# Performance work log

Measured on AMD Instinct MI355X. Metric: run time of the kernel, lower is better.

The kernel has to match this reference:

```python
import jax, jax.numpy as jnp
import numpy as np

N_HEADS = 8

def setup_inputs() -> dict:
    key = jax.random.key(0)
    qkv = jax.random.normal(key, (4, 1536, 2048), dtype=jnp.float32)
    return {"qkv": qkv}

def reference(qkv):
    bs, width, length = qkv.shape
    ch = width // (3 * N_HEADS)
    q, k, v = jnp.split(qkv, 3, axis=1)  # each [bs, H*C, T]
    scale = 1.0 / np.sqrt(ch).astype(np.float32)
    q = (q * scale).reshape(bs * N_HEADS, ch, length)
    k = k.reshape(bs * N_HEADS, ch, length)
    v = v.reshape(bs * N_HEADS, ch, length)
    weight = jnp.einsum('bct,bcs->bts', q, k)  # [bs*H, T, T]
    weight = jax.nn.softmax(weight.astype(jnp.float32), axis=-1).astype(weight.dtype)
    a = jnp.einsum('bts,bcs->bct', weight, v)  # [bs*H, C, T]
    return a.reshape(bs, -1, length)
```

## Files before the change

kernel.cpp:

```cpp
#include <hip/hip_runtime.h>
#include <hip/hip_bf16.h>

typedef unsigned short u16;
typedef unsigned int uint;
typedef __bf16 bf16x8 __attribute__((ext_vector_type(8)));
typedef float f32x16 __attribute__((ext_vector_type(16)));

#define SEQ 2048
#define DH  64

__device__ __forceinline__ u16 f2bf(float x) {
  __bf16 h = (__bf16)x;
  return __builtin_bit_cast(u16, h);
}

#define FSW(r) ((((r) & 3) << 1) | (((r) >> 2) & 1))

__global__ __launch_bounds__(256) void transpose_qk(const float* __restrict__ qkv,
                                                    u16* __restrict__ qT,
                                                    u16* __restrict__ kT) {
  int idx = blockIdx.x;
  int which = idx >> 10;
  int bh = (idx >> 5) & 31;
  int t0 = (idx & 31) * 64;
  int b = bh >> 3, h = bh & 7;
  const float* src = qkv + ((size_t)(b*1536 + which*512 + h*64)) * SEQ;
  u16* dst = (which ? kT : qT) + (size_t)bh * SEQ * DH;
  float scale = which ? 1.0f : 0.1803368801111244f;

  __shared__ float tile[64][65];
  int tl = threadIdx.x & 63;
  int cw = threadIdx.x >> 6;
#pragma unroll
  for (int i = 0; i < 16; ++i) {
    int c = cw + 4*i;
    tile[c][tl] = src[(size_t)c*SEQ + t0 + tl] * scale;
  }
  __syncthreads();
  int cl2 = (threadIdx.x & 31) * 2;
  int tw  = threadIdx.x >> 5;
#pragma unroll
  for (int i = 0; i < 8; ++i) {
    int t = tw + 8*i;
    unsigned int lo = f2bf(tile[cl2][t]);
    unsigned int hi = f2bf(tile[cl2+1][t]);
    *(unsigned int*)(dst + (size_t)(t0 + t)*DH + cl2) = lo | (hi << 16);
  }
}

__global__ __launch_bounds__(256) void convert_v(const float* __restrict__ qkv,
                                                 u16* __restrict__ v) {
  int row = blockIdx.x;
  int bh = row >> 6, c = row & 63;
  int b = bh >> 3, h = bh & 7;
  const float4* src = (const float4*)(qkv + ((size_t)(b*1536 + 1024 + h*64 + c)) * SEQ);
  u16* dst = v + (size_t)row * SEQ;
  int tid = threadIdx.x;
  float4 a = src[tid*2];
  float4 bq = src[tid*2+1];
  union { u16 u[8]; int4 v4; } pk;
  pk.u[0]=f2bf(a.x); pk.u[1]=f2bf(a.y); pk.u[2]=f2bf(a.z); pk.u[3]=f2bf(a.w);
  pk.u[4]=f2bf(bq.x); pk.u[5]=f2bf(bq.y); pk.u[6]=f2bf(bq.z); pk.u[7]=f2bf(bq.w);
  *(int4*)(dst + tid*8) = pk.v4;
}

__global__ __launch_bounds__(256) void attn(const u16* __restrict__ qT,
                                            const u16* __restrict__ kT,
                                            const u16* __restrict__ vB,
                                            float* __restrict__ out) {
  const int lb = (blockIdx.x & 7) * 64 + (blockIdx.x >> 3);
  const int bh = lb >> 4;
  const int t0 = (lb & 15) * 128;
  const int tid  = threadIdx.x;
  const int wave = tid >> 6;
  const int lane = tid & 63;
  const int l31  = lane & 31;
  const int hi   = lane >> 5;

  __shared__ __align__(16) u16 kbuf[2][2][64*64];
  __shared__ __align__(16) u16 vbuf[2][2][64*64];

  const u16* qrow = qT + ((size_t)bh*SEQ + (t0 + wave*32 + l31)) * DH;
  bf16x8 bq[4];
#pragma unroll
  for (int kb = 0; kb < 4; ++kb) bq[kb] = *(const bf16x8*)(qrow + kb*16 + hi*8);

  const u16* ksrc0 = kT + (size_t)bh*SEQ*DH;
  const u16* vsrc0 = vB + (size_t)bh*DH*SEQ;
  const int ci0 = (wave*2+0)*64 + lane;
  const int ci1 = (wave*2+1)*64 + lane;
  const int kr0 = ci0 >> 3, kc0 = ci0 & 7;
  const int kr1 = ci1 >> 3, kc1 = ci1 & 7;
  const u16* kg0 = ksrc0 + (size_t)kr0*DH + ((kc0 ^ FSW(kr0)) * 8);
  const u16* kg1 = ksrc0 + (size_t)kr1*DH + ((kc1 ^ FSW(kr1)) * 8);
  const u16* vg0 = vsrc0 + (size_t)kr0*SEQ + ((kc0 ^ FSW(kr0)) * 8);
  const u16* vg1 = vsrc0 + (size_t)kr1*SEQ + ((kc1 ^ FSW(kr1)) * 8);

#define GLDS(src, dst) __builtin_amdgcn_global_load_lds(                        \
    (const __attribute__((address_space(1))) unsigned int*)(src),               \
    (__attribute__((address_space(3))) unsigned int*)(dst), 16, 0, 0)
#define STAGE(b, h, sbase) do {                                                 \
    GLDS(kg0 + (size_t)((sbase) + (h)*64)*DH, &kbuf[b][h][ci0*8]);              \
    GLDS(kg1 + (size_t)((sbase) + (h)*64)*DH, &kbuf[b][h][ci1*8]);              \
    GLDS(vg0 + ((sbase) + (h)*64),            &vbuf[b][h][ci0*8]);              \
    GLDS(vg1 + ((sbase) + (h)*64),            &vbuf[b][h][ci1*8]);              \
  } while (0)

  f32x16 acc0 = {}, acc1 = {};
  float l_run = 0.f;
  const int fl = FSW(l31);

  STAGE(0, 0, 0); STAGE(0, 1, 0);
  __syncthreads();

  int buf = 0;
  for (int s0 = 0; s0 < SEQ; s0 += 128) {
    if (s0 + 128 < SEQ) { STAGE(buf ^ 1, 0, s0 + 128); STAGE(buf ^ 1, 1, s0 + 128); }

#pragma unroll
    for (int half = 0; half < 2; ++half) {
      const u16* kb_ = &kbuf[buf][half][0];
      const u16* vb_ = &vbuf[buf][half][0];

      f32x16 S0 = {}, S1 = {};
      __builtin_amdgcn_s_setprio(1);
#pragma unroll
      for (int kb = 0; kb < 4; ++kb) {
        bf16x8 a0 = *(const bf16x8*)(kb_ + l31*64      + (((2*kb+hi) ^ fl) * 8));
        bf16x8 a1 = *(const bf16x8*)(kb_ + (32+l31)*64 + (((2*kb+hi) ^ fl) * 8));
        S0 = __builtin_amdgcn_mfma_f32_32x32x16_bf16(a0, bq[kb], S0, 0, 0, 0);
        S1 = __builtin_amdgcn_mfma_f32_32x32x16_bf16(a1, bq[kb], S1, 0, 0, 0);
      }
      __builtin_amdgcn_s_setprio(0);

      float p0[16], p1[16];
#pragma unroll
      for (int i = 0; i < 16; ++i) p0[i] = __builtin_amdgcn_exp2f(S0[i]);
#pragma unroll
      for (int i = 0; i < 16; ++i) p1[i] = __builtin_amdgcn_exp2f(S1[i]);

      float sm[16];
#pragma unroll
      for (int i = 0; i < 16; ++i) sm[i] = p0[i] + p1[i];
#pragma unroll
      for (int i = 0; i < 8; ++i) sm[i] += sm[i+8];
#pragma unroll
      for (int i = 0; i < 4; ++i) sm[i] += sm[i+4];
      float ls = (sm[0] + sm[1]) + (sm[2] + sm[3]);
      ls += __shfl_xor(ls, 32);
      l_run += ls;

      uint d0[8], d1[8];
#pragma unroll
      for (int q = 0; q < 4; ++q)
#pragma unroll
        for (int e = 0; e < 2; ++e) {
          asm("v_cvt_pk_bf16_f32 %0, %1, %2" : "=v"(d0[2*q+e]) : "v"(p0[4*q+2*e]), "v"(p0[4*q+2*e+1]));
          asm("v_cvt_pk_bf16_f32 %0, %1, %2" : "=v"(d1[2*q+e]) : "v"(p1[4*q+2*e]), "v"(p1[4*q+2*e+1]));
        }
      bf16x8 pf[4];
#pragma unroll
      for (int st2 = 0; st2 < 2; ++st2)
#pragma unroll
        for (int kb2 = 0; kb2 < 2; ++kb2) {
          uint X0 = (st2 ? d1 : d0)[4*kb2+0], X1 = (st2 ? d1 : d0)[4*kb2+1];
          uint Y0 = (st2 ? d1 : d0)[4*kb2+2], Y1 = (st2 ? d1 : d0)[4*kb2+3];
          asm("v_permlane32_swap_b32 %0, %1" : "+v"(X0), "+v"(Y0));
          asm("v_permlane32_swap_b32 %0, %1" : "+v"(X1), "+v"(Y1));
          uint4 u = {X0, X1, Y0, Y1};
          pf[st2*2+kb2] = __builtin_bit_cast(bf16x8, u);
        }

      __builtin_amdgcn_s_setprio(1);
#pragma unroll
      for (int ks = 0; ks < 4; ++ks) {
        bf16x8 a0 = *(const bf16x8*)(vb_ + l31*64      + (((2*ks+hi) ^ fl) * 8));
        bf16x8 a1 = *(const bf16x8*)(vb_ + (32+l31)*64 + (((2*ks+hi) ^ fl) * 8));
        acc0 = __builtin_amdgcn_mfma_f32_32x32x16_bf16(a0, pf[ks], acc0, 0, 0, 0);
        acc1 = __builtin_amdgcn_mfma_f32_32x32x16_bf16(a1, pf[ks], acc1, 0, 0, 0);
      }
      __builtin_amdgcn_s_setprio(0);
    }

    __syncthreads();
    buf ^= 1;
  }
#undef STAGE
#undef GLDS

  float linv = 1.0f / l_run;
  float* ob = out + (size_t)(bh*64) * SEQ + t0 + wave*32 + l31;
#pragma unroll
  for (int r = 0; r < 16; ++r) {
    int c0 = (r & 3) + 8*(r >> 2) + 4*hi;
    ob[(size_t)c0 * SEQ]        = acc0[r] * linv;
    ob[(size_t)(32 + c0) * SEQ] = acc1[r] * linv;
  }
}

extern "C" void kernel_launch(void* const* d_in, const int* in_sizes, int n_in,
                              void* d_out, int out_size, void* d_ws, size_t ws_size,
                              hipStream_t stream) {
  const float* qkv = (const float*)d_in[0];
  float* out = (float*)d_out;
  u16* qT = (u16*)d_ws;
  u16* kT = qT + (size_t)32*SEQ*DH;
  u16* vB = kT + (size_t)32*SEQ*DH;
  transpose_qk<<<2048, 256, 0, stream>>>(qkv, qT, kT);
  convert_v<<<2048, 256, 0, stream>>>(qkv, vB);
  attn<<<512, 256, 0, stream>>>(qT, kT, vB, out);
}
```

Measured before the change: 64.59 us.

## Split key dimension across wave pairs with 2x2 query/channel tiles and LDS reduction

Reorganizes the attention work so each pair of waves owns 64 query rows, and each wave in the pair handles half of every 64-key sub-tile. Each K and V fragment loaded from LDS now feeds two MFMAs instead of one, which halves LDS read traffic per MFMA. At the end, partial accumulators and row sums are combined through shared memory. The cost is four accumulators per wave, which raises register pressure, plus an extra epilogue reduction and barrier in which only half the waves write output.

```diff
diff --git a/kernel.cpp b/kernel.cpp
--- a/kernel.cpp
+++ b/kernel.cpp
@@ -73,17 +73,21 @@
   const int t0 = (lb & 15) * 128;
   const int tid  = threadIdx.x;
   const int wave = tid >> 6;
+  const int th   = wave >> 1;
+  const int sh   = wave & 1;
   const int lane = tid & 63;
   const int l31  = lane & 31;
   const int hi   = lane >> 5;
 
-  __shared__ __align__(16) u16 kbuf[2][2][64*64];
-  __shared__ __align__(16) u16 vbuf[2][2][64*64];
-
-  const u16* qrow = qT + ((size_t)bh*SEQ + (t0 + wave*32 + l31)) * DH;
-  bf16x8 bq[4];
-#pragma unroll
-  for (int kb = 0; kb < 4; ++kb) bq[kb] = *(const bf16x8*)(qrow + kb*16 + hi*8);
+  __shared__ __align__(16) u16 smem[2][2][2][64*64];
+
+  const u16* qrow = qT + ((size_t)bh*SEQ + (t0 + th*64 + l31)) * DH;
+  bf16x8 bq[2][4];
+#pragma unroll
+  for (int tb = 0; tb < 2; ++tb)
+#pragma unroll
+    for (int kb = 0; kb < 4; ++kb)
+      bq[tb][kb] = *(const bf16x8*)(qrow + (size_t)tb*32*DH + kb*16 + hi*8);
 
   const u16* ksrc0 = kT + (size_t)bh*SEQ*DH;
   const u16* vsrc0 = vB + (size_t)bh*DH*SEQ;
@@ -100,14 +104,14 @@
     (const __attribute__((address_space(1))) unsigned int*)(src),               \
     (__attribute__((address_space(3))) unsigned int*)(dst), 16, 0, 0)
 #define STAGE(b, h, sbase) do {                                                 \
-    GLDS(kg0 + (size_t)((sbase) + (h)*64)*DH, &kbuf[b][h][ci0*8]);              \
-    GLDS(kg1 + (size_t)((sbase) + (h)*64)*DH, &kbuf[b][h][ci1*8]);              \
-    GLDS(vg0 + ((sbase) + (h)*64),            &vbuf[b][h][ci0*8]);              \
-    GLDS(vg1 + ((sbase) + (h)*64),            &vbuf[b][h][ci1*8]);              \
+    GLDS(kg0 + (size_t)((sbase) + (h)*64)*DH, &smem[b][h][0][ci0*8]);           \
+    GLDS(kg1 + (size_t)((sbase) + (h)*64)*DH, &smem[b][h][0][ci1*8]);           \
+    GLDS(vg0 + ((sbase) + (h)*64),            &smem[b][h][1][ci0*8]);           \
+    GLDS(vg1 + ((sbase) + (h)*64),            &smem[b][h][1][ci1*8]);           \
   } while (0)
 
-  f32x16 acc0 = {}, acc1 = {};
-  float l_run = 0.f;
+  f32x16 acc00 = {}, acc01 = {}, acc10 = {}, acc11 = {};
+  float l_run0 = 0.f, l_run1 = 0.f;
   const int fl = FSW(l31);
 
   STAGE(0, 0, 0); STAGE(0, 1, 0);
@@ -119,17 +123,16 @@
 
 #pragma unroll
     for (int half = 0; half < 2; ++half) {
-      const u16* kb_ = &kbuf[buf][half][0];
-      const u16* vb_ = &vbuf[buf][half][0];
+      const u16* kb_ = &smem[buf][half][0][0];
+      const u16* vb_ = &smem[buf][half][1][0];
 
       f32x16 S0 = {}, S1 = {};
       __builtin_amdgcn_s_setprio(1);
 #pragma unroll
       for (int kb = 0; kb < 4; ++kb) {
-        bf16x8 a0 = *(const bf16x8*)(kb_ + l31*64      + (((2*kb+hi) ^ fl) * 8));
-        bf16x8 a1 = *(const bf16x8*)(kb_ + (32+l31)*64 + (((2*kb+hi) ^ fl) * 8));
-        S0 = __builtin_amdgcn_mfma_f32_32x32x16_bf16(a0, bq[kb], S0, 0, 0, 0);
-        S1 = __builtin_amdgcn_mfma_f32_32x32x16_bf16(a1, bq[kb], S1, 0, 0, 0);
+        bf16x8 a = *(const bf16x8*)(kb_ + (sh*32 + l31)*64 + (((2*kb+hi) ^ fl) * 8));
+        S0 = __builtin_amdgcn_mfma_f32_32x32x16_bf16(a, bq[0][kb], S0, 0, 0, 0);
+        S1 = __builtin_amdgcn_mfma_f32_32x32x16_bf16(a, bq[1][kb], S1, 0, 0, 0);
       }
       __builtin_amdgcn_s_setprio(0);
 
@@ -139,16 +142,30 @@
 #pragma unroll
       for (int i = 0; i < 16; ++i) p1[i] = __builtin_amdgcn_exp2f(S1[i]);
 
-      float sm[16];
-#pragma unroll
-      for (int i = 0; i < 16; ++i) sm[i] = p0[i] + p1[i];
-#pragma unroll
-      for (int i = 0; i < 8; ++i) sm[i] += sm[i+8];
-#pragma unroll
-      for (int i = 0; i < 4; ++i) sm[i] += sm[i+4];
-      float ls = (sm[0] + sm[1]) + (sm[2] + sm[3]);
-      ls += __shfl_xor(ls, 32);
-      l_run += ls;
+      {
+        float sm[16];
+#pragma unroll
+        for (int i = 0; i < 16; ++i) sm[i] = p0[i];
+#pragma unroll
+        for (int i = 0; i < 8; ++i) sm[i] += sm[i+8];
+#pragma unroll
+        for (int i = 0; i < 4; ++i) sm[i] += sm[i+4];
+        float ls = (sm[0] + sm[1]) + (sm[2] + sm[3]);
+        ls += __shfl_xor(ls, 32);
+        l_run0 += ls;
+      }
+      {
+        float sm[16];
+#pragma unroll
+        for (int i = 0; i < 16; ++i) sm[i] = p1[i];
+#pragma unroll
+        for (int i = 0; i < 8; ++i) sm[i] += sm[i+8];
+#pragma unroll
+        for (int i = 0; i < 4; ++i) sm[i] += sm[i+4];
+        float ls = (sm[0] + sm[1]) + (sm[2] + sm[3]);
+        ls += __shfl_xor(ls, 32);
+        l_run1 += ls;
+      }
 
       uint d0[8], d1[8];
 #pragma unroll
@@ -158,26 +175,28 @@
           asm("v_cvt_pk_bf16_f32 %0, %1, %2" : "=v"(d0[2*q+e]) : "v"(p0[4*q+2*e]), "v"(p0[4*q+2*e+1]));
           asm("v_cvt_pk_bf16_f32 %0, %1, %2" : "=v"(d1[2*q+e]) : "v"(p1[4*q+2*e]), "v"(p1[4*q+2*e+1]));
         }
-      bf16x8 pf[4];
-#pragma unroll
-      for (int st2 = 0; st2 < 2; ++st2)
+      bf16x8 pf[2][2];
+#pragma unroll
+      for (int tb2 = 0; tb2 < 2; ++tb2)
 #pragma unroll
         for (int kb2 = 0; kb2 < 2; ++kb2) {
-          uint X0 = (st2 ? d1 : d0)[4*kb2+0], X1 = (st2 ? d1 : d0)[4*kb2+1];
-          uint Y0 = (st2 ? d1 : d0)[4*kb2+2], Y1 = (st2 ? d1 : d0)[4*kb2+3];
+          uint X0 = (tb2 ? d1 : d0)[4*kb2+0], X1 = (tb2 ? d1 : d0)[4*kb2+1];
+          uint Y0 = (tb2 ? d1 : d0)[4*kb2+2], Y1 = (tb2 ? d1 : d0)[4*kb2+3];
           asm("v_permlane32_swap_b32 %0, %1" : "+v"(X0), "+v"(Y0));
           asm("v_permlane32_swap_b32 %0, %1" : "+v"(X1), "+v"(Y1));
           uint4 u = {X0, X1, Y0, Y1};
-          pf[st2*2+kb2] = __builtin_bit_cast(bf16x8, u);
+          pf[tb2][kb2] = __builtin_bit_cast(bf16x8, u);
         }
 
       __builtin_amdgcn_s_setprio(1);
 #pragma unroll
-      for (int ks = 0; ks < 4; ++ks) {
-        bf16x8 a0 = *(const bf16x8*)(vb_ + l31*64      + (((2*ks+hi) ^ fl) * 8));
-        bf16x8 a1 = *(const bf16x8*)(vb_ + (32+l31)*64 + (((2*ks+hi) ^ fl) * 8));
-        acc0 = __builtin_amdgcn_mfma_f32_32x32x16_bf16(a0, pf[ks], acc0, 0, 0, 0);
-        acc1 = __builtin_amdgcn_mfma_f32_32x32x16_bf16(a1, pf[ks], acc1, 0, 0, 0);
+      for (int ks2 = 0; ks2 < 2; ++ks2) {
+        bf16x8 av0 = *(const bf16x8*)(vb_ + l31*64      + (((sh*4 + ks2*2 + hi) ^ fl) * 8));
+        bf16x8 av1 = *(const bf16x8*)(vb_ + (32+l31)*64 + (((sh*4 + ks2*2 + hi) ^ fl) * 8));
+        acc00 = __builtin_amdgcn_mfma_f32_32x32x16_bf16(av0, pf[0][ks2], acc00, 0, 0, 0);
+        acc01 = __builtin_amdgcn_mfma_f32_32x32x16_bf16(av0, pf[1][ks2], acc01, 0, 0, 0);
+        acc10 = __builtin_amdgcn_mfma_f32_32x32x16_bf16(av1, pf[0][ks2], acc10, 0, 0, 0);
+        acc11 = __builtin_amdgcn_mfma_f32_32x32x16_bf16(av1, pf[1][ks2], acc11, 0, 0, 0);
       }
       __builtin_amdgcn_s_setprio(0);
     }
@@ -188,13 +207,47 @@
 #undef STAGE
 #undef GLDS
 
-  float linv = 1.0f / l_run;
-  float* ob = out + (size_t)(bh*64) * SEQ + t0 + wave*32 + l31;
-#pragma unroll
-  for (int r = 0; r < 16; ++r) {
-    int c0 = (r & 3) + 8*(r >> 2) + 4*hi;
-    ob[(size_t)c0 * SEQ]        = acc0[r] * linv;
-    ob[(size_t)(32 + c0) * SEQ] = acc1[r] * linv;
+  float* ep = (float*)&smem[0][0][0][0];
+  float* lp = ep + 8*1024;
+  if (sh == 1) {
+#pragma unroll
+    for (int cb = 0; cb < 2; ++cb)
+#pragma unroll
+      for (int tb = 0; tb < 2; ++tb) {
+        const f32x16* a = (cb == 0) ? (tb == 0 ? &acc00 : &acc01)
+                                    : (tb == 0 ? &acc10 : &acc11);
+        float* base = ep + (th*4 + cb*2 + tb)*1024 + lane;
+#pragma unroll
+        for (int r = 0; r < 16; ++r) base[r*64] = (*a)[r];
+      }
+    lp[(th*2+0)*64 + lane] = l_run0;
+    lp[(th*2+1)*64 + lane] = l_run1;
+  }
+  __syncthreads();
+  if (sh == 0) {
+#pragma unroll
+    for (int cb = 0; cb < 2; ++cb)
+#pragma unroll
+      for (int tb = 0; tb < 2; ++tb) {
+        f32x16* a = (cb == 0) ? (tb == 0 ? &acc00 : &acc01)
+                              : (tb == 0 ? &acc10 : &acc11);
+        const float* base = ep + (th*4 + cb*2 + tb)*1024 + lane;
+#pragma unroll
+        for (int r = 0; r < 16; ++r) (*a)[r] += base[r*64];
+      }
+    float lt0 = l_run0 + lp[(th*2+0)*64 + lane];
+    float lt1 = l_run1 + lp[(th*2+1)*64 + lane];
+    float linv0 = 1.0f / lt0;
+    float linv1 = 1.0f / lt1;
+    float* ob = out + (size_t)(bh*64) * SEQ + t0 + th*64 + l31;
+#pragma unroll
+    for (int r = 0; r < 16; ++r) {
+      int c0 = (r & 3) + 8*(r >> 2) + 4*hi;
+      ob[(size_t)c0 * SEQ]             = acc00[r] * linv0;
+      ob[(size_t)c0 * SEQ + 32]        = acc01[r] * linv1;
+      ob[(size_t)(32 + c0) * SEQ]      = acc10[r] * linv0;
+      ob[(size_t)(32 + c0) * SEQ + 32] = acc11[r] * linv1;
+    }
   }
 }
 
```

Result: slower. 65.89 us (+2.0%).

## Split key dimension across wave pairs with LDS reduction, halve query tile

Applied to the files above, without the earlier changes.

The attention kernel now gives each block 64 queries instead of 128. Its four waves are arranged as two query halves times two key halves, and each wave handles 32 keys per 64-key stage. Partial accumulators and row sums are reduced through shared memory at the end. The grid doubles to 1024 blocks, shared memory is halved and launch bounds request 4 blocks per CU, to improve occupancy and CU fill on the 256-CU part. The costs are twice as many K/V tile loads per query, more barriers per key, and an extra LDS reduction epilogue.

```diff
diff --git a/kernel.cpp b/kernel.cpp
--- a/kernel.cpp
+++ b/kernel.cpp
@@ -64,23 +64,24 @@
   *(int4*)(dst + tid*8) = pk.v4;
 }
 
-__global__ __launch_bounds__(256) void attn(const u16* __restrict__ qT,
-                                            const u16* __restrict__ kT,
-                                            const u16* __restrict__ vB,
-                                            float* __restrict__ out) {
-  const int lb = (blockIdx.x & 7) * 64 + (blockIdx.x >> 3);
-  const int bh = lb >> 4;
-  const int t0 = (lb & 15) * 128;
+__global__ __launch_bounds__(256, 4) void attn(const u16* __restrict__ qT,
+                                               const u16* __restrict__ kT,
+                                               const u16* __restrict__ vB,
+                                               float* __restrict__ out) {
+  const int lb = (blockIdx.x & 7) * 128 + (blockIdx.x >> 3);
+  const int bh = lb >> 5;
+  const int t0 = (lb & 31) * 64;
   const int tid  = threadIdx.x;
   const int wave = tid >> 6;
+  const int th   = wave & 1;
+  const int sh   = wave >> 1;
   const int lane = tid & 63;
   const int l31  = lane & 31;
   const int hi   = lane >> 5;
 
-  __shared__ __align__(16) u16 kbuf[2][2][64*64];
-  __shared__ __align__(16) u16 vbuf[2][2][64*64];
-
-  const u16* qrow = qT + ((size_t)bh*SEQ + (t0 + wave*32 + l31)) * DH;
+  __shared__ __align__(16) u16 smem[2][2][64*64];
+
+  const u16* qrow = qT + ((size_t)bh*SEQ + (t0 + th*32 + l31)) * DH;
   bf16x8 bq[4];
 #pragma unroll
   for (int kb = 0; kb < 4; ++kb) bq[kb] = *(const bf16x8*)(qrow + kb*16 + hi*8);
@@ -99,88 +100,77 @@
 #define GLDS(src, dst) __builtin_amdgcn_global_load_lds(                        \
     (const __attribute__((address_space(1))) unsigned int*)(src),               \
     (__attribute__((address_space(3))) unsigned int*)(dst), 16, 0, 0)
-#define STAGE(b, h, sbase) do {                                                 \
-    GLDS(kg0 + (size_t)((sbase) + (h)*64)*DH, &kbuf[b][h][ci0*8]);              \
-    GLDS(kg1 + (size_t)((sbase) + (h)*64)*DH, &kbuf[b][h][ci1*8]);              \
-    GLDS(vg0 + ((sbase) + (h)*64),            &vbuf[b][h][ci0*8]);              \
-    GLDS(vg1 + ((sbase) + (h)*64),            &vbuf[b][h][ci1*8]);              \
+#define STAGE(b, sbase) do {                                                    \
+    GLDS(kg0 + (size_t)(sbase)*DH, &smem[b][0][ci0*8]);                         \
+    GLDS(kg1 + (size_t)(sbase)*DH, &smem[b][0][ci1*8]);                         \
+    GLDS(vg0 + (sbase),            &smem[b][1][ci0*8]);                         \
+    GLDS(vg1 + (sbase),            &smem[b][1][ci1*8]);                         \
   } while (0)
 
   f32x16 acc0 = {}, acc1 = {};
   float l_run = 0.f;
   const int fl = FSW(l31);
 
-  STAGE(0, 0, 0); STAGE(0, 1, 0);
+  STAGE(0, 0);
   __syncthreads();
 
   int buf = 0;
-  for (int s0 = 0; s0 < SEQ; s0 += 128) {
-    if (s0 + 128 < SEQ) { STAGE(buf ^ 1, 0, s0 + 128); STAGE(buf ^ 1, 1, s0 + 128); }
-
-#pragma unroll
-    for (int half = 0; half < 2; ++half) {
-      const u16* kb_ = &kbuf[buf][half][0];
-      const u16* vb_ = &vbuf[buf][half][0];
-
-      f32x16 S0 = {}, S1 = {};
-      __builtin_amdgcn_s_setprio(1);
-#pragma unroll
-      for (int kb = 0; kb < 4; ++kb) {
-        bf16x8 a0 = *(const bf16x8*)(kb_ + l31*64      + (((2*kb+hi) ^ fl) * 8));
-        bf16x8 a1 = *(const bf16x8*)(kb_ + (32+l31)*64 + (((2*kb+hi) ^ fl) * 8));
-        S0 = __builtin_amdgcn_mfma_f32_32x32x16_bf16(a0, bq[kb], S0, 0, 0, 0);
-        S1 = __builtin_amdgcn_mfma_f32_32x32x16_bf16(a1, bq[kb], S1, 0, 0, 0);
-      }
-      __builtin_amdgcn_s_setprio(0);
-
-      float p0[16], p1[16];
-#pragma unroll
-      for (int i = 0; i < 16; ++i) p0[i] = __builtin_amdgcn_exp2f(S0[i]);
-#pragma unroll
-      for (int i = 0; i < 16; ++i) p1[i] = __builtin_amdgcn_exp2f(S1[i]);
-
-      float sm[16];
-#pragma unroll
-      for (int i = 0; i < 16; ++i) sm[i] = p0[i] + p1[i];
-#pragma unroll
-      for (int i = 0; i < 8; ++i) sm[i] += sm[i+8];
+  for (int s0 = 0; s0 < SEQ; s0 += 64) {
+    if (s0 + 64 < SEQ) STAGE(buf ^ 1, s0 + 64);
+
+    const u16* kb_ = &smem[buf][0][0];
+    const u16* vb_ = &smem[buf][1][0];
+
+    f32x16 S0 = {};
+    __builtin_amdgcn_s_setprio(1);
+#pragma unroll
+    for (int kb = 0; kb < 4; ++kb) {
+      bf16x8 a = *(const bf16x8*)(kb_ + (sh*32 + l31)*64 + (((2*kb+hi) ^ fl) * 8));
+      S0 = __builtin_amdgcn_mfma_f32_32x32x16_bf16(a, bq[kb], S0, 0, 0, 0);
+    }
+    __builtin_amdgcn_s_setprio(0);
+
+    float p0[16];
+#pragma unroll
+    for (int i = 0; i < 16; ++i) p0[i] = __builtin_amdgcn_exp2f(S0[i]);
+    {
+      float sm[8];
+#pragma unroll
+      for (int i = 0; i < 8; ++i) sm[i] = p0[i] + p0[i+8];
 #pragma unroll
       for (int i = 0; i < 4; ++i) sm[i] += sm[i+4];
       float ls = (sm[0] + sm[1]) + (sm[2] + sm[3]);
       ls += __shfl_xor(ls, 32);
       l_run += ls;
-
-      uint d0[8], d1[8];
-#pragma unroll
-      for (int q = 0; q < 4; ++q)
-#pragma unroll
-        for (int e = 0; e < 2; ++e) {
-          asm("v_cvt_pk_bf16_f32 %0, %1, %2" : "=v"(d0[2*q+e]) : "v"(p0[4*q+2*e]), "v"(p0[4*q+2*e+1]));
-          asm("v_cvt_pk_bf16_f32 %0, %1, %2" : "=v"(d1[2*q+e]) : "v"(p1[4*q+2*e]), "v"(p1[4*q+2*e+1]));
-        }
-      bf16x8 pf[4];
-#pragma unroll
-      for (int st2 = 0; st2 < 2; ++st2)
-#pragma unroll
-        for (int kb2 = 0; kb2 < 2; ++kb2) {
-          uint X0 = (st2 ? d1 : d0)[4*kb2+0], X1 = (st2 ? d1 : d0)[4*kb2+1];
-          uint Y0 = (st2 ? d1 : d0)[4*kb2+2], Y1 = (st2 ? d1 : d0)[4*kb2+3];
-          asm("v_permlane32_swap_b32 %0, %1" : "+v"(X0), "+v"(Y0));
-          asm("v_permlane32_swap_b32 %0, %1" : "+v"(X1), "+v"(Y1));
-          uint4 u = {X0, X1, Y0, Y1};
-          pf[st2*2+kb2] = __builtin_bit_cast(bf16x8, u);
-        }
-
-      __builtin_amdgcn_s_setprio(1);
-#pragma unroll
-      for (int ks = 0; ks < 4; ++ks) {
-        bf16x8 a0 = *(const bf16x8*)(vb_ + l31*64      + (((2*ks+hi) ^ fl) * 8));
-        bf16x8 a1 = *(const bf16x8*)(vb_ + (32+l31)*64 + (((2*ks+hi) ^ fl) * 8));
-        acc0 = __builtin_amdgcn_mfma_f32_32x32x16_bf16(a0, pf[ks], acc0, 0, 0, 0);
-        acc1 = __builtin_amdgcn_mfma_f32_32x32x16_bf16(a1, pf[ks], acc1, 0, 0, 0);
+    }
+
+    uint d0[8];
+#pragma unroll
+    for (int q = 0; q < 4; ++q)
+#pragma unroll
+      for (int e = 0; e < 2; ++e) {
+        asm("v_cvt_pk_bf16_f32 %0, %1, %2" : "=v"(d0[2*q+e]) : "v"(p0[4*q+2*e]), "v"(p0[4*q+2*e+1]));
       }
-      __builtin_amdgcn_s_setprio(0);
-    }
+    bf16x8 pf[2];
+#pragma unroll
+    for (int kb2 = 0; kb2 < 2; ++kb2) {
+      uint X0 = d0[4*kb2+0], X1 = d0[4*kb2+1];
+      uint Y0 = d0[4*kb2+2], Y1 = d0[4*kb2+3];
+      asm("v_permlane32_swap_b32 %0, %1" : "+v"(X0), "+v"(Y0));
+      asm("v_permlane32_swap_b32 %0, %1" : "+v"(X1), "+v"(Y1));
+      uint4 u = {X0, X1, Y0, Y1};
+      pf[kb2] = __builtin_bit_cast(bf16x8, u);
+    }
+
+    __builtin_amdgcn_s_setprio(1);
+#pragma unroll
+    for (int ks2 = 0; ks2 < 2; ++ks2) {
+      bf16x8 av0 = *(const bf16x8*)(vb_ + l31*64      + (((sh*4 + ks2*2 + hi) ^ fl) * 8));
+      bf16x8 av1 = *(const bf16x8*)(vb_ + (32+l31)*64 + (((sh*4 + ks2*2 + hi) ^ fl) * 8));
+      acc0 = __builtin_amdgcn_mfma_f32_32x32x16_bf16(av0, pf[ks2], acc0, 0, 0, 0);
+      acc1 = __builtin_amdgcn_mfma_f32_32x32x16_bf16(av1, pf[ks2], acc1, 0, 0, 0);
+    }
+    __builtin_amdgcn_s_setprio(0);
 
     __syncthreads();
     buf ^= 1;
@@ -188,13 +178,30 @@
 #undef STAGE
 #undef GLDS
 
-  float linv = 1.0f / l_run;
-  float* ob = out + (size_t)(bh*64) * SEQ + t0 + wave*32 + l31;
-#pragma unroll
-  for (int r = 0; r < 16; ++r) {
-    int c0 = (r & 3) + 8*(r >> 2) + 4*hi;
-    ob[(size_t)c0 * SEQ]        = acc0[r] * linv;
-    ob[(size_t)(32 + c0) * SEQ] = acc1[r] * linv;
+  float* ep = (float*)&smem[0][0][0];
+  float* lp = ep + 4*1024;
+  if (sh == 1) {
+    float* b0 = ep + (th*2+0)*1024 + lane;
+    float* b1 = ep + (th*2+1)*1024 + lane;
+#pragma unroll
+    for (int r = 0; r < 16; ++r) { b0[r*64] = acc0[r]; b1[r*64] = acc1[r]; }
+    lp[th*64 + lane] = l_run;
+  }
+  __syncthreads();
+  if (sh == 0) {
+    const float* b0 = ep + (th*2+0)*1024 + lane;
+    const float* b1 = ep + (th*2+1)*1024 + lane;
+#pragma unroll
+    for (int r = 0; r < 16; ++r) { acc0[r] += b0[r*64]; acc1[r] += b1[r*64]; }
+    float lt = l_run + lp[th*64 + lane];
+    float linv = 1.0f / lt;
+    float* ob = out + (size_t)(bh*64) * SEQ + t0 + th*32 + l31;
+#pragma unroll
+    for (int r = 0; r < 16; ++r) {
+      int c0 = (r & 3) + 8*(r >> 2) + 4*hi;
+      ob[(size_t)c0 * SEQ]        = acc0[r] * linv;
+      ob[(size_t)(32 + c0) * SEQ] = acc1[r] * linv;
+    }
   }
 }
 
@@ -208,5 +215,5 @@
   u16* vB = kT + (size_t)32*SEQ*DH;
   transpose_qk<<<2048, 256, 0, stream>>>(qkv, qT, kT);
   convert_v<<<2048, 256, 0, stream>>>(qkv, vB);
-  attn<<<512, 256, 0, stream>>>(qT, kT, vB, out);
-}
+  attn<<<1024, 256, 0, stream>>>(qT, kT, vB, out);
+}
```

After: 65.56 us. About the same (+1.5%).
